# Optimization experiments

Hardware: AMD Instinct MI355X
Metric: run time of the kernel (lower is better)

The kernel has to match this reference:

```python
import jax, jax.numpy as jnp
import numpy as np

B, L, FT, FS, H = 32, 4096, 512, 512, 512  # batch, seq, text feat, summary feat, hidden
C = FT + FS + 1  # conv1 in-channels (num_features + 1 coverage channel)


def setup_inputs() -> dict:
    key = jax.random.key(0)
    ks = jax.random.split(key, 8)
    text_states = jax.random.normal(ks[0], (B, L, FT), dtype=jnp.float32)
    summary_current_state = jax.random.normal(ks[1], (B, FS), dtype=jnp.float32)
    coverage = jax.random.uniform(ks[2], (B, 1, L), dtype=jnp.float32)
    W1 = jax.random.normal(ks[3], (H, C), dtype=jnp.float32) * (1.0 / np.sqrt(C))
    b1 = jnp.zeros((H,), dtype=jnp.float32)
    W2 = jax.random.normal(ks[4], (1, H), dtype=jnp.float32) * (1.0 / np.sqrt(H))
    b2 = jnp.zeros((1,), dtype=jnp.float32)
    text_length = jax.random.randint(ks[5], (B,), 1, L + 1)  # >=1 so softmax is defined
    return {
        "text_states": text_states,
        "summary_current_state": summary_current_state,
        "coverage": coverage,
        "W1": W1,
        "b1": b1,
        "W2": W2,
        "b2": b2,
        "text_length": text_length,
    }


def reference(text_states, summary_current_state, coverage, W1, b1, W2, b2, text_length):
    b, l, ft = text_states.shape
    ts = jnp.swapaxes(text_states, -1, -2)  # [B, FT, L]
    ss = jnp.broadcast_to(summary_current_state[..., None],
                          summary_current_state.shape + (l,))  # [B, FS, L]
    x = jnp.concatenate([ts, ss, coverage], axis=-2)  # [B, C, L]
    # kernel-size-1 Conv1d == pointwise linear over channels
    h = jnp.tanh(jnp.einsum('bcl,hc->bhl', x, W1) + b1[None, :, None])  # [B, H, L]
    logits = jnp.einsum('bhl,oh->bol', h, W2) + b2[None, :, None]  # [B, 1, L]
    mask = jnp.arange(l)[None, None, :] < text_length[:, None, None]  # [B, 1, L]
    masked = jnp.where(mask, logits, -jnp.inf)
    attention = jax.nn.softmax(masked, axis=-1)  # [B, 1, L]
    context_vector = jnp.sum(attention * ts, axis=-1)  # [B, FT]
    return context_vector, attention
```

## Files before the change

### kernel.cpp

```cpp
#include <hip/hip_runtime.h>
#include <cstdint>
#include <cstddef>

#define B_  32
#define L_  4096
#define FT_ 512
#define FS_ 512
#define H_  512
#define C_  1025

typedef __attribute__((ext_vector_type(8))) short short8;
typedef __attribute__((ext_vector_type(4))) float float4v;

__device__ __forceinline__ short f2bf(float f) {
    union { float f; unsigned u; } v; v.f = f;
    unsigned r = v.u + 0x7FFF + ((v.u >> 16) & 1);
    return (short)(r >> 16);
}

__device__ __forceinline__ float fast_tanh(float x) {
    float e = __expf(2.f * x);
    return 1.f - 2.f * __builtin_amdgcn_rcpf(e + 1.f);
}

__global__ __launch_bounds__(256) void prep_kernel(
        const float* __restrict__ W1, const float* __restrict__ summary,
        const float* __restrict__ b1, short* __restrict__ fragB,
        float* __restrict__ w1c, float* __restrict__ sconst) {
    if (blockIdx.x < 128) {
        int gid = blockIdx.x * 256 + threadIdx.x;
        int lane = gid & 63;
        int ts_  = gid >> 6;
        int t = ts_ >> 4;
        int s = ts_ & 15;
        int h  = t * 16 + (lane & 15);
        int k0 = s * 32 + (lane >> 4) * 8;
        const float* src = W1 + (size_t)h * C_ + k0;
        short8 o;
        #pragma unroll
        for (int j = 0; j < 8; ++j) o[j] = f2bf(src[j]);
        *(short8*)(fragB + (size_t)gid * 8) = o;
        if (gid < H_) w1c[gid] = W1[(size_t)gid * C_ + FT_ + FS_];
    } else {
        int wid  = ((blockIdx.x - 128) * 256 + threadIdx.x) >> 6;
        int lane = threadIdx.x & 63;
        int b = wid >> 9;
        int h = wid & 511;
        const float* wrow = W1 + (size_t)h * C_ + FT_;
        const float* srow = summary + (size_t)b * FS_;
        float acc = 0.f;
        #pragma unroll
        for (int f = lane; f < FS_; f += 64) acc += wrow[f] * srow[f];
        #pragma unroll
        for (int off = 32; off > 0; off >>= 1) acc += __shfl_down(acc, off, 64);
        if (lane == 0) sconst[wid] = acc + b1[h];
    }
}

#define TL 32
__global__ __launch_bounds__(256, 4) void logits_kernel(
        const float* __restrict__ ts, const float* __restrict__ coverage,
        const int* __restrict__ text_length,
        const short* __restrict__ fragB, const float* __restrict__ w1c,
        const float* __restrict__ sconst, const float* __restrict__ W2,
        const float* __restrict__ b2, float* __restrict__ logits) {
    const int b  = blockIdx.y;
    const int l0 = blockIdx.x * TL;
    const int len = text_length[b];
    if (l0 >= len) return;

    __shared__ short ts_lds[TL * 512];

    const float4* src = (const float4*)(ts + ((size_t)b * L_ + l0) * FT_);
    for (int j = threadIdx.x; j < TL * 64; j += 256) {
        int l = j >> 6;
        int g = j & 63;
        float4 v0 = src[2 * j];
        float4 v1 = src[2 * j + 1];
        short8 p;
        p[0] = f2bf(v0.x); p[1] = f2bf(v0.y); p[2] = f2bf(v0.z); p[3] = f2bf(v0.w);
        p[4] = f2bf(v1.x); p[5] = f2bf(v1.y); p[6] = f2bf(v1.z); p[7] = f2bf(v1.w);
        *(short8*)(ts_lds + l * 512 + ((g ^ (l & 7)) << 3)) = p;
    }
    __syncthreads();

    const int lane = threadIdx.x & 63;
    const int wv   = threadIdx.x >> 6;
    const int col  = lane & 15;
    const int quad = lane >> 4;
    const int swz  = col & 7;

    const short* aBase = ts_lds + col * 512;
    const short* bBase = fragB + (size_t)(wv * 8) * 16 * 512 + lane * 8;

    float4v acc[8][2];
    #pragma unroll
    for (int nt = 0; nt < 8; ++nt)
        #pragma unroll
        for (int mt = 0; mt < 2; ++mt)
            acc[nt][mt] = (float4v){0.f, 0.f, 0.f, 0.f};

    #pragma unroll 2
    for (int ks = 0; ks < 16; ++ks) {
        short8 af[2];
        const int ag = ((ks * 4 + quad) ^ swz) << 3;
        #pragma unroll
        for (int mt = 0; mt < 2; ++mt)
            af[mt] = *(const short8*)(aBase + mt * (16 * 512) + ag);
        #pragma unroll
        for (int nt = 0; nt < 8; ++nt) {
            short8 bf = *(const short8*)(bBase + (size_t)(nt * 16 + ks) * 512);
            #pragma unroll
            for (int mt = 0; mt < 2; ++mt)
                acc[nt][mt] = __builtin_amdgcn_mfma_f32_16x16x32_bf16(
                    af[mt], bf, acc[nt][mt], 0, 0, 0);
        }
    }

    const int h0 = wv * 128;
    const float* sc_b = sconst + (size_t)b * H_;
    float4 cov[2];
    #pragma unroll
    for (int mt = 0; mt < 2; ++mt)
        cov[mt] = *(const float4*)(coverage + (size_t)b * L_ + l0 + mt * 16 + quad * 4);

    float partial[2][4];
    #pragma unroll
    for (int mt = 0; mt < 2; ++mt)
        #pragma unroll
        for (int r = 0; r < 4; ++r) partial[mt][r] = 0.f;

    #pragma unroll
    for (int nt = 0; nt < 8; ++nt) {
        const int h = h0 + nt * 16 + col;
        const float sc = sc_b[h];
        const float wc = w1c[h];
        const float w2 = W2[h];
        #pragma unroll
        for (int mt = 0; mt < 2; ++mt)
            #pragma unroll
            for (int r = 0; r < 4; ++r) {
                float pre = acc[nt][mt][r] + sc + wc * ((const float*)&cov[mt])[r];
                partial[mt][r] += w2 * fast_tanh(pre);
            }
    }

    #pragma unroll
    for (int mt = 0; mt < 2; ++mt)
        #pragma unroll
        for (int r = 0; r < 4; ++r) {
            float v = partial[mt][r];
            v += __shfl_xor(v, 8, 64);
            v += __shfl_xor(v, 4, 64);
            v += __shfl_xor(v, 2, 64);
            v += __shfl_xor(v, 1, 64);
            partial[mt][r] = v;
        }

    __syncthreads();
    float* red = (float*)ts_lds;
    if (col == 0) {
        #pragma unroll
        for (int mt = 0; mt < 2; ++mt)
            #pragma unroll
            for (int r = 0; r < 4; ++r)
                red[wv * 32 + mt * 16 + quad * 4 + r] = partial[mt][r];
    }
    __syncthreads();
    if (threadIdx.x < 32) {
        const int lg = l0 + threadIdx.x;
        if (lg < len) {
            float s = b2[0];
            #pragma unroll
            for (int w = 0; w < 4; ++w) s += red[w * 32 + threadIdx.x];
            logits[(size_t)b * L_ + lg] = s;
        }
    }
}

__global__ __launch_bounds__(1024) void softmax_stats_kernel(
        const float* __restrict__ logits, const int* __restrict__ text_length,
        float2* __restrict__ stats) {
    const int b = blockIdx.x;
    const int len = text_length[b];
    const float* lg = logits + (size_t)b * L_;
    __shared__ float sred[1024];

    float m = -INFINITY;
    for (int l = threadIdx.x; l < len; l += 1024) m = fmaxf(m, lg[l]);
    sred[threadIdx.x] = m;
    __syncthreads();
    for (int s = 512; s > 0; s >>= 1) {
        if (threadIdx.x < s)
            sred[threadIdx.x] = fmaxf(sred[threadIdx.x], sred[threadIdx.x + s]);
        __syncthreads();
    }
    m = sred[0];
    __syncthreads();

    float sum = 0.f;
    for (int l = threadIdx.x; l < len; l += 1024) sum += __expf(lg[l] - m);
    sred[threadIdx.x] = sum;
    __syncthreads();
    for (int s = 512; s > 0; s >>= 1) {
        if (threadIdx.x < s) sred[threadIdx.x] += sred[threadIdx.x + s];
        __syncthreads();
    }
    if (threadIdx.x == 0) {
        float2 st; st.x = m; st.y = 1.f / sred[0];
        stats[b] = st;
    }
}

#define LC 128
__global__ __launch_bounds__(256) void context_kernel(
        const float* __restrict__ ts, const float* __restrict__ logits,
        const float2* __restrict__ stats, const int* __restrict__ text_length,
        float* __restrict__ attn_out, float* __restrict__ cpart) {
    const int b = blockIdx.y;
    const int c = blockIdx.x;
    const int l0 = c * LC;
    const int len = text_length[b];
    const float2 st = stats[b];

    __shared__ float a_s[LC];
    if (threadIdx.x < LC) {
        const int l = l0 + threadIdx.x;
        float a = 0.f;
        if (l < len) a = __expf(logits[(size_t)b * L_ + l] - st.x) * st.y;
        a_s[threadIdx.x] = a;
        attn_out[(size_t)b * L_ + l] = a;
    }
    __syncthreads();

    const int lpar = threadIdx.x >> 7;
    const int f4   = threadIdx.x & 127;
    float4 acc = {0.f, 0.f, 0.f, 0.f};
    if (l0 < len) {
        const int lend = min(len - l0, LC);
        const float4* row = (const float4*)(ts + ((size_t)b * L_ + l0 + lpar) * FT_) + f4;
        for (int i = lpar; i < lend; i += 2, row += 256) {
            const float a = a_s[i];
            float4 v = *row;
            acc.x += a * v.x; acc.y += a * v.y;
            acc.z += a * v.z; acc.w += a * v.w;
        }
    }
    ((float4*)cpart)[(size_t)((b * 32 + c) * 2 + lpar) * 128 + f4] = acc;
}

__global__ __launch_bounds__(128) void context_reduce_kernel(
        const float* __restrict__ cpart, float* __restrict__ ctx) {
    const int b = blockIdx.x;
    const int t = threadIdx.x;
    float4 s = {0.f, 0.f, 0.f, 0.f};
    const float4* p = (const float4*)cpart + (size_t)b * 64 * 128 + t;
    #pragma unroll
    for (int c = 0; c < 64; ++c) {
        float4 v = p[c * 128];
        s.x += v.x; s.y += v.y; s.z += v.z; s.w += v.w;
    }
    ((float4*)ctx)[(size_t)b * 128 + t] = s;
}

extern "C" void kernel_launch(void* const* d_in, const int* in_sizes, int n_in,
                              void* d_out, int out_size, void* d_ws, size_t ws_size,
                              hipStream_t stream) {
    const float* ts       = (const float*)d_in[0];
    const float* summary  = (const float*)d_in[1];
    const float* coverage = (const float*)d_in[2];
    const float* W1       = (const float*)d_in[3];
    const float* b1       = (const float*)d_in[4];
    const float* W2       = (const float*)d_in[5];
    const float* b2       = (const float*)d_in[6];
    const int*   text_len = (const int*)d_in[7];

    float* ctx_out  = (float*)d_out;
    float* attn_out = (float*)d_out + B_ * FT_;

    char* ws = (char*)d_ws;
    short*  fragB  = (short*)(ws);
    float*  w1c    = (float*)(ws + 524288);
    float*  sconst = (float*)(ws + 526336);
    float*  logits = (float*)(ws + 591872);
    float2* stats  = (float2*)(ws + 1116160);
    float*  cpart  = (float*)(ws + 1116672);

    prep_kernel<<<128 + 4096, 256, 0, stream>>>(W1, summary, b1, fragB, w1c, sconst);
    logits_kernel<<<dim3(L_ / TL, B_), 256, 0, stream>>>(
        ts, coverage, text_len, fragB, w1c, sconst, W2, b2, logits);
    softmax_stats_kernel<<<B_, 1024, 0, stream>>>(logits, text_len, stats);
    context_kernel<<<dim3(L_ / LC, B_), 256, 0, stream>>>(
        ts, logits, stats, text_len, attn_out, cpart);
    context_reduce_kernel<<<B_, 128, 0, stream>>>(cpart, ctx_out);
}
```

Baseline: 420.1 us.

## Fuse softmax and context accumulation into logits kernel with online-softmax chunk stats

```diff
diff --git a/kernel.cpp b/kernel.cpp
--- a/kernel.cpp
+++ b/kernel.cpp
@@ -8,6 +8,8 @@
 #define FS_ 512
 #define H_  512
 #define C_  1025
+#define TL  32
+#define NCH (L_ / TL)
 
 typedef __attribute__((ext_vector_type(8))) short short8;
 typedef __attribute__((ext_vector_type(4))) float float4v;
@@ -57,13 +59,13 @@
     }
 }
 
-#define TL 32
-__global__ __launch_bounds__(256, 4) void logits_kernel(
+__global__ __launch_bounds__(256, 4) void logits_ctx_kernel(
         const float* __restrict__ ts, const float* __restrict__ coverage,
         const int* __restrict__ text_length,
         const short* __restrict__ fragB, const float* __restrict__ w1c,
         const float* __restrict__ sconst, const float* __restrict__ W2,
-        const float* __restrict__ b2, float* __restrict__ logits) {
+        const float* __restrict__ b2, float* __restrict__ logits,
+        float2* __restrict__ stats_c, float* __restrict__ cpart) {
     const int b  = blockIdx.y;
     const int l0 = blockIdx.x * TL;
     const int len = text_length[b];
@@ -158,7 +160,8 @@
         }
 
     __syncthreads();
-    float* red = (float*)ts_lds;
+    float* red  = (float*)ts_lds;
+    float* wbuf = red + 128;
     if (col == 0) {
         #pragma unroll
         for (int mt = 0; mt < 2; ++mt)
@@ -167,100 +170,99 @@
                 red[wv * 32 + mt * 16 + quad * 4 + r] = partial[mt][r];
     }
     __syncthreads();
-    if (threadIdx.x < 32) {
-        const int lg = l0 + threadIdx.x;
-        if (lg < len) {
-            float s = b2[0];
-            #pragma unroll
-            for (int w = 0; w < 4; ++w) s += red[w * 32 + threadIdx.x];
-            logits[(size_t)b * L_ + lg] = s;
-        }
-    }
-}
-
-__global__ __launch_bounds__(1024) void softmax_stats_kernel(
-        const float* __restrict__ logits, const int* __restrict__ text_length,
-        float2* __restrict__ stats) {
-    const int b = blockIdx.x;
+
+    if (threadIdx.x < 64) {
+        const int t = threadIdx.x;
+        float lg = 0.f;
+        const bool valid = (t < 32) && (l0 + t < len);
+        if (t < 32) {
+            lg = b2[0];
+            #pragma unroll
+            for (int w = 0; w < 4; ++w) lg += red[w * 32 + t];
+            logits[(size_t)b * L_ + l0 + t] = lg;
+        }
+        float mv = valid ? lg : -INFINITY;
+        #pragma unroll
+        for (int off = 32; off > 0; off >>= 1)
+            mv = fmaxf(mv, __shfl_xor(mv, off, 64));
+        const float wt = valid ? __expf(lg - mv) : 0.f;
+        float sv = wt;
+        #pragma unroll
+        for (int off = 32; off > 0; off >>= 1) sv += __shfl_xor(sv, off, 64);
+        if (t < 32) wbuf[t] = wt;
+        if (t == 0) {
+            float2 o; o.x = mv; o.y = sv;
+            stats_c[(size_t)b * NCH + blockIdx.x] = o;
+        }
+    }
+    __syncthreads();
+
+    const int lend = min(len - l0, TL);
+    const float* tsbase = ts + ((size_t)b * L_ + l0) * FT_ + 2 * threadIdx.x;
+    float cx = 0.f, cy = 0.f;
+    for (int l = 0; l < lend; ++l) {
+        const float wl = wbuf[l];
+        const float2 v = *(const float2*)(tsbase + (size_t)l * FT_);
+        cx += wl * v.x; cy += wl * v.y;
+    }
+    float2 o; o.x = cx; o.y = cy;
+    *(float2*)(cpart + ((size_t)b * NCH + blockIdx.x) * FT_ + 2 * threadIdx.x) = o;
+}
+
+__global__ __launch_bounds__(512) void finalize_kernel(
+        const float* __restrict__ logits, const float2* __restrict__ stats_c,
+        const float* __restrict__ cpart, const int* __restrict__ text_length,
+        float* __restrict__ ctx, float* __restrict__ attn_out) {
+    const int b   = blockIdx.x;
     const int len = text_length[b];
-    const float* lg = logits + (size_t)b * L_;
-    __shared__ float sred[1024];
-
-    float m = -INFINITY;
-    for (int l = threadIdx.x; l < len; l += 1024) m = fmaxf(m, lg[l]);
-    sred[threadIdx.x] = m;
-    __syncthreads();
-    for (int s = 512; s > 0; s >>= 1) {
-        if (threadIdx.x < s)
-            sred[threadIdx.x] = fmaxf(sred[threadIdx.x], sred[threadIdx.x + s]);
-        __syncthreads();
-    }
-    m = sred[0];
-    __syncthreads();
-
-    float sum = 0.f;
-    for (int l = threadIdx.x; l < len; l += 1024) sum += __expf(lg[l] - m);
-    sred[threadIdx.x] = sum;
-    __syncthreads();
-    for (int s = 512; s > 0; s >>= 1) {
-        if (threadIdx.x < s) sred[threadIdx.x] += sred[threadIdx.x + s];
-        __syncthreads();
-    }
-    if (threadIdx.x == 0) {
-        float2 st; st.x = m; st.y = 1.f / sred[0];
-        stats[b] = st;
-    }
-}
-
-#define LC 128
-__global__ __launch_bounds__(256) void context_kernel(
-        const float* __restrict__ ts, const float* __restrict__ logits,
-        const float2* __restrict__ stats, const int* __restrict__ text_length,
-        float* __restrict__ attn_out, float* __restrict__ cpart) {
-    const int b = blockIdx.y;
-    const int c = blockIdx.x;
-    const int l0 = c * LC;
-    const int len = text_length[b];
-    const float2 st = stats[b];
-
-    __shared__ float a_s[LC];
-    if (threadIdx.x < LC) {
-        const int l = l0 + threadIdx.x;
+    const int nv  = (len + TL - 1) / TL;
+    const int t   = threadIdx.x;
+    __shared__ float sm[NCH];
+    __shared__ float redm[8];
+    __shared__ float reds[8];
+
+    float2 st; st.x = 0.f; st.y = 0.f;
+    float mloc = -INFINITY;
+    if (t < nv) { st = stats_c[(size_t)b * NCH + t]; mloc = st.x; }
+    float v = mloc;
+    #pragma unroll
+    for (int off = 32; off > 0; off >>= 1) v = fmaxf(v, __shfl_xor(v, off, 64));
+    if ((t & 63) == 0) redm[t >> 6] = v;
+    __syncthreads();
+    float m = redm[0];
+    #pragma unroll
+    for (int w = 1; w < 8; ++w) m = fmaxf(m, redm[w]);
+
+    float sume = 0.f;
+    if (t < nv) {
+        const float sc = __expf(st.x - m);
+        sm[t] = sc;
+        sume = st.y * sc;
+    }
+    float sv = sume;
+    #pragma unroll
+    for (int off = 32; off > 0; off >>= 1) sv += __shfl_xor(sv, off, 64);
+    if ((t & 63) == 0) reds[t >> 6] = sv;
+    __syncthreads();
+    float tot = 0.f;
+    #pragma unroll
+    for (int w = 0; w < 8; ++w) tot += reds[w];
+    const float inv = 1.f / tot;
+
+    const float* lgrow = logits + (size_t)b * L_;
+    float* arow = attn_out + (size_t)b * L_;
+    #pragma unroll
+    for (int i = 0; i < L_ / 512; ++i) {
+        const int l = i * 512 + t;
         float a = 0.f;
-        if (l < len) a = __expf(logits[(size_t)b * L_ + l] - st.x) * st.y;
-        a_s[threadIdx.x] = a;
-        attn_out[(size_t)b * L_ + l] = a;
-    }
-    __syncthreads();
-
-    const int lpar = threadIdx.x >> 7;
-    const int f4   = threadIdx.x & 127;
-    float4 acc = {0.f, 0.f, 0.f, 0.f};
-    if (l0 < len) {
-        const int lend = min(len - l0, LC);
-        const float4* row = (const float4*)(ts + ((size_t)b * L_ + l0 + lpar) * FT_) + f4;
-        for (int i = lpar; i < lend; i += 2, row += 256) {
-            const float a = a_s[i];
-            float4 v = *row;
-            acc.x += a * v.x; acc.y += a * v.y;
-            acc.z += a * v.z; acc.w += a * v.w;
-        }
-    }
-    ((float4*)cpart)[(size_t)((b * 32 + c) * 2 + lpar) * 128 + f4] = acc;
-}
-
-__global__ __launch_bounds__(128) void context_reduce_kernel(
-        const float* __restrict__ cpart, float* __restrict__ ctx) {
-    const int b = blockIdx.x;
-    const int t = threadIdx.x;
-    float4 s = {0.f, 0.f, 0.f, 0.f};
-    const float4* p = (const float4*)cpart + (size_t)b * 64 * 128 + t;
-    #pragma unroll
-    for (int c = 0; c < 64; ++c) {
-        float4 v = p[c * 128];
-        s.x += v.x; s.y += v.y; s.z += v.z; s.w += v.w;
-    }
-    ((float4*)ctx)[(size_t)b * 128 + t] = s;
+        if (l < len) a = __expf(lgrow[l] - m) * inv;
+        arow[l] = a;
+    }
+
+    const float* cp = cpart + (size_t)b * NCH * FT_ + t;
+    float c = 0.f;
+    for (int ch = 0; ch < nv; ++ch) c += sm[ch] * cp[(size_t)ch * FT_];
+    ctx[(size_t)b * FT_ + t] = c * inv;
 }
 
 extern "C" void kernel_launch(void* const* d_in, const int* in_sizes, int n_in,
@@ -279,18 +281,16 @@
     float* attn_out = (float*)d_out + B_ * FT_;
 
     char* ws = (char*)d_ws;
-    short*  fragB  = (short*)(ws);
-    float*  w1c    = (float*)(ws + 524288);
-    float*  sconst = (float*)(ws + 526336);
-    float*  logits = (float*)(ws + 591872);
-    float2* stats  = (float2*)(ws + 1116160);
-    float*  cpart  = (float*)(ws + 1116672);
+    short*  fragB   = (short*)(ws);
+    float*  w1c     = (float*)(ws + 524288);
+    float*  sconst  = (float*)(ws + 526336);
+    float*  logits  = (float*)(ws + 591872);
+    float2* stats_c = (float2*)(ws + 1116160);
+    float*  cpart   = (float*)(ws + 1148928);
 
     prep_kernel<<<128 + 4096, 256, 0, stream>>>(W1, summary, b1, fragB, w1c, sconst);
-    logits_kernel<<<dim3(L_ / TL, B_), 256, 0, stream>>>(
-        ts, coverage, text_len, fragB, w1c, sconst, W2, b2, logits);
-    softmax_stats_kernel<<<B_, 1024, 0, stream>>>(logits, text_len, stats);
-    context_kernel<<<dim3(L_ / LC, B_), 256, 0, stream>>>(
-        ts, logits, stats, text_len, attn_out, cpart);
-    context_reduce_kernel<<<B_, 128, 0, stream>>>(cpart, ctx_out);
-}
+    logits_ctx_kernel<<<dim3(NCH, B_), 256, 0, stream>>>(
+        ts, coverage, text_len, fragB, w1c, sconst, W2, b2, logits, stats_c, cpart);
+    finalize_kernel<<<B_, 512, 0, stream>>>(
+        logits, stats_c, cpart, text_len, ctx_out, attn_out);
+}
```

Result: faster. 411.2 us (-2.1%).
